# Kernel optimization log

Hardware: AMD Instinct MI355X
Metric: run time of the kernel (lower is better)

The kernel has to match this reference:

```python
import jax, jax.numpy as jnp
import numpy as np

HEAD_NUM = 16
EMBED_DIM = 512


def setup_inputs() -> dict:
    key = jax.random.key(0)
    k1, k2, k3, k4, k5 = jax.random.split(key, 5)
    B, N, D = 8, 2048, EMBED_DIM
    x = jax.random.normal(k1, (B, N, D), dtype=jnp.float32)
    dis_matrix = jax.random.uniform(k2, (B, N, N), dtype=jnp.float32)
    s = 1.0 / np.sqrt(D)
    Wq = jax.random.normal(k3, (D, D), dtype=jnp.float32) * s
    Wk = jax.random.normal(k4, (D, D), dtype=jnp.float32) * s
    Wv = jax.random.normal(k5, (D, D), dtype=jnp.float32) * s
    alpha = jnp.float32(1.0)
    return {"x": x, "dis_matrix": dis_matrix, "Wq": Wq, "Wk": Wk, "Wv": Wv, "alpha": alpha}


def _split_heads(t, H):
    # [B, N, D] -> [B, H, N, D//H]
    B, N, D = t.shape
    return t.reshape(B, N, H, D // H).transpose(0, 2, 1, 3)


def reference(x, dis_matrix, Wq, Wk, Wv, alpha):
    B, N, D = x.shape
    H = HEAD_NUM
    # nn.Linear(bias=False): y = x @ W.T
    q = _split_heads(x @ Wq.T, H)  # [B,H,N,dk]
    k = _split_heads(x @ Wk.T, H)
    v = _split_heads(x @ Wv.T, H)
    log2n = jnp.float32(np.log2(N))
    dis_weight = jnp.exp(-alpha * log2n * dis_matrix)  # [B,N,N]
    k_weight = jnp.exp(k)
    # contract over source node i -> target node j
    weight_1 = jnp.einsum('bij,bhik->bhjk', dis_weight, k_weight * v)
    weight_2 = jnp.einsum('bij,bhik->bhjk', dis_weight, k_weight)
    out = jax.nn.sigmoid(q) * (weight_1 / weight_2)  # [B,H,N,dk]
    return out.transpose(0, 2, 1, 3).reshape(B, N, D)
```

## Files before the change

kernel.cpp:

```cpp
#include <hip/hip_runtime.h>
#include <math.h>
#include <stdint.h>


typedef __bf16 bf16_t;
typedef __attribute__((ext_vector_type(4))) __bf16 bf16x4;
typedef __attribute__((ext_vector_type(8))) __bf16 bf16x8;
typedef __attribute__((ext_vector_type(4))) float f32x4;

#define MFMA_BF16(a, b, c) __builtin_amdgcn_mfma_f32_16x16x32_bf16((a), (b), (c), 0, 0, 0)

static __device__ __forceinline__ void async_ld16(const bf16_t* g, bf16_t* lds) {
  __builtin_amdgcn_global_load_lds(
      reinterpret_cast<__attribute__((address_space(1))) unsigned int*>(
          reinterpret_cast<uintptr_t>(g)),
      reinterpret_cast<__attribute__((address_space(3))) unsigned int*>(
          reinterpret_cast<uintptr_t>(lds)),
      16, 0, 0);
}

template <int BK, int ROWS>
static __device__ __forceinline__ void stage(const bf16_t* g, int ldg, bf16_t* lds,
                                             int wv, int lane) {
  constexpr int CH = BK / 8;
  constexpr int RPW = 64 / CH;
  const int r_in = lane / CH;
  const int cpos = lane % CH;
#pragma unroll
  for (int s = 0; s < ROWS / (RPW * 4); ++s) {
    int rbase = wv * (ROWS / 4) + s * RPW;
    int row = rbase + r_in;
    int cg = cpos ^ ((row >> 1) & 3);
    async_ld16(g + (size_t)row * ldg + cg * 8, lds + rbase * BK + lane * 8);
  }
}

template <int BK>
static __device__ __forceinline__ bf16x8 frag_read(const bf16_t* lds, int row16,
                                                   int l15, int quad, int kc) {
  int p = (quad ^ ((l15 >> 1) & 3)) + kc * 4;
  return *(const bf16x8*)&lds[(row16 + l15) * BK + p * 8];
}

__global__ __launch_bounds__(256) void cvt_all(const float* __restrict__ x,
                                               const float* __restrict__ wq,
                                               const float* __restrict__ wk,
                                               const float* __restrict__ wv,
                                               bf16_t* __restrict__ xb,
                                               bf16_t* __restrict__ wall) {
  int i = blockIdx.x * 256 + threadIdx.x;
  if (i >= 2293760) return;
  const float* src;
  bf16_t* dst;
  int off;
  if (i < 2097152) {
    src = x; dst = xb; off = i;
  } else {
    int j = i - 2097152;
    int sel = j >> 16;
    off = j & 65535;
    src = (sel == 0) ? wq : (sel == 1) ? wk : wv;
    dst = wall + (size_t)sel * 262144;
  }
  f32x4 f = ((const f32x4*)src)[off];
  bf16x4 o;
  o[0] = (bf16_t)f[0]; o[1] = (bf16_t)f[1]; o[2] = (bf16_t)f[2]; o[3] = (bf16_t)f[3];
  ((bf16x4*)dst)[off] = o;
}

__global__ __launch_bounds__(256, 4) void proj_gemm(const bf16_t* __restrict__ A,
                                                    const bf16_t* __restrict__ W,
                                                    bf16_t* __restrict__ qs,
                                                    bf16_t* __restrict__ kwT,
                                                    bf16_t* __restrict__ kwvT) {
  __shared__ __align__(16) char pool[17408];
  bf16_t* As = (bf16_t*)pool;
  const int K = 512;
  const int tid = threadIdx.x;
  const int wv = tid >> 6, lane = tid & 63;
  const int l15 = lane & 15, quad = lane >> 4;
  const int m_blk = blockIdx.x, n_blk = blockIdx.y;
  const int wm = wv >> 1, wn = wv & 1;
  const bf16_t* Am = A + (size_t)(m_blk * 128) * K;

  if (n_blk < 4) {
    bf16_t* Bsq = (bf16_t*)(pool + 8192);
    const int c_loc = n_blk * 128;
    f32x4 acc[4][4];
#pragma unroll
    for (int a = 0; a < 4; ++a)
#pragma unroll
      for (int b = 0; b < 4; ++b) acc[a][b] = (f32x4){0.f, 0.f, 0.f, 0.f};

    for (int k0 = 0; k0 < K; k0 += 32) {
      stage<32, 128>(Am + k0, K, As, wv, lane);
      stage<32, 128>(W + (size_t)c_loc * K + k0, K, Bsq, wv, lane);
      __syncthreads();
      bf16x8 a[4], bb[4];
#pragma unroll
      for (int mf = 0; mf < 4; ++mf) a[mf] = frag_read<32>(As, wm * 64 + mf * 16, l15, quad, 0);
#pragma unroll
      for (int nf = 0; nf < 4; ++nf) bb[nf] = frag_read<32>(Bsq, wn * 64 + nf * 16, l15, quad, 0);
#pragma unroll
      for (int mf = 0; mf < 4; ++mf)
#pragma unroll
        for (int nf = 0; nf < 4; ++nf) acc[mf][nf] = MFMA_BF16(a[mf], bb[nf], acc[mf][nf]);
      __syncthreads();
    }
#pragma unroll
    for (int mf = 0; mf < 4; ++mf)
#pragma unroll
      for (int nf = 0; nf < 4; ++nf) {
        int c = c_loc + wn * 64 + nf * 16 + l15;
#pragma unroll
        for (int r = 0; r < 4; ++r) {
          int t = m_blk * 128 + wm * 64 + mf * 16 + quad * 4 + r;
          qs[(size_t)t * 512 + c] = (bf16_t)(1.0f / (1.0f + __expf(-acc[mf][nf][r])));
        }
      }
  } else {
    bf16_t* Bk = (bf16_t*)(pool + 8192);
    bf16_t* Bv = (bf16_t*)(pool + 12288);
    const int c_loc = (n_blk - 4) * 64;
    f32x4 acck[4][2], accv[4][2];
#pragma unroll
    for (int a = 0; a < 4; ++a)
#pragma unroll
      for (int b = 0; b < 2; ++b) {
        acck[a][b] = (f32x4){0.f, 0.f, 0.f, 0.f};
        accv[a][b] = (f32x4){0.f, 0.f, 0.f, 0.f};
      }
    const bf16_t* Wk = W + (size_t)(512 + c_loc) * K;
    const bf16_t* Wv = W + (size_t)(1024 + c_loc) * K;

    for (int k0 = 0; k0 < K; k0 += 32) {
      stage<32, 128>(Am + k0, K, As, wv, lane);
      stage<32, 64>(Wk + k0, K, Bk, wv, lane);
      stage<32, 64>(Wv + k0, K, Bv, wv, lane);
      __syncthreads();
      bf16x8 a[4], bk[2], bv[2];
#pragma unroll
      for (int mf = 0; mf < 4; ++mf) a[mf] = frag_read<32>(As, wm * 64 + mf * 16, l15, quad, 0);
#pragma unroll
      for (int nf = 0; nf < 2; ++nf) {
        bk[nf] = frag_read<32>(Bk, wn * 32 + nf * 16, l15, quad, 0);
        bv[nf] = frag_read<32>(Bv, wn * 32 + nf * 16, l15, quad, 0);
      }
#pragma unroll
      for (int mf = 0; mf < 4; ++mf)
#pragma unroll
        for (int nf = 0; nf < 2; ++nf) {
          acck[mf][nf] = MFMA_BF16(a[mf], bk[nf], acck[mf][nf]);
          accv[mf][nf] = MFMA_BF16(a[mf], bv[nf], accv[mf][nf]);
        }
      __syncthreads();
    }

    bf16_t* Lk = (bf16_t*)pool;
    bf16_t* Lv = (bf16_t*)(pool + 8704);
    const int bb = m_blk >> 4;
    const int t0 = (m_blk * 128) & 2047;
#pragma unroll
    for (int ci = 0; ci < 2; ++ci) {
      if (wn == ci) {
#pragma unroll
        for (int mf = 0; mf < 4; ++mf)
#pragma unroll
          for (int nf = 0; nf < 2; ++nf) {
            int cl = nf * 16 + l15;
            int tl = wm * 64 + mf * 16 + quad * 4;
#pragma unroll
            for (int r = 0; r < 4; ++r) {
              float kw = __expf(acck[mf][nf][r]);
              Lk[cl * 136 + tl + r] = (bf16_t)kw;
              Lv[cl * 136 + tl + r] = (bf16_t)(kw * accv[mf][nf][r]);
            }
          }
      }
      __syncthreads();
      {
        int rowt = tid >> 3, colt = (tid & 7) * 16;
        int c = c_loc + ci * 32 + rowt;
        size_t g = ((size_t)bb * 512 + c) * 2048 + t0 + colt;
        *(bf16x8*)&kwT[g] = *(const bf16x8*)&Lk[rowt * 136 + colt];
        *(bf16x8*)&kwT[g + 8] = *(const bf16x8*)&Lk[rowt * 136 + colt + 8];
        *(bf16x8*)&kwvT[g] = *(const bf16x8*)&Lv[rowt * 136 + colt];
        *(bf16x8*)&kwvT[g + 8] = *(const bf16x8*)&Lv[rowt * 136 + colt + 8];
      }
      __syncthreads();
    }
  }
}

__global__ __launch_bounds__(256) void make_dwT(const float* __restrict__ dis,
                                                bf16_t* __restrict__ dwT,
                                                const float* __restrict__ alpha) {
  __shared__ bf16_t t[64 * 65];
  const float coef = -alpha[0] * 11.0f;
  const int j0 = blockIdx.x * 64, i0 = blockIdx.y * 64, b = blockIdx.z;
  const int tid = threadIdx.x;
  const int rr = tid >> 4, cc = (tid & 15) * 4;
#pragma unroll
  for (int p = 0; p < 4; ++p) {
    int i = rr + p * 16;
    f32x4 d = *(const f32x4*)&dis[((size_t)(b * 2048 + i0 + i)) * 2048 + j0 + cc];
#pragma unroll
    for (int e = 0; e < 4; ++e) t[(cc + e) * 65 + i] = (bf16_t)__expf(coef * d[e]);
  }
  __syncthreads();
#pragma unroll
  for (int p = 0; p < 4; ++p) {
    int j = rr + p * 16;
    bf16x4 o;
#pragma unroll
    for (int e = 0; e < 4; ++e) o[e] = t[j * 65 + cc + e];
    *(bf16x4*)&dwT[((size_t)(b * 2048 + j0 + j)) * 2048 + i0 + cc] = o;
  }
}

__global__ __launch_bounds__(256, 4) void main_gemm(const bf16_t* __restrict__ dwT,
                                                    const bf16_t* __restrict__ kwvT,
                                                    const bf16_t* __restrict__ kwT,
                                                    const bf16_t* __restrict__ qs,
                                                    float* __restrict__ out) {
  __shared__ bf16_t As[128 * 64];
  __shared__ bf16_t Bs[128 * 64];
  const int K = 2048;
  const int tid = threadIdx.x;
  const int wv = tid >> 6, lane = tid & 63;
  const int l15 = lane & 15, quad = lane >> 4;
  const int i = blockIdx.x;
  const int b = i & 7, nb = (i >> 3) & 7, mb = i >> 6;
  const int wm = wv >> 1, wn = wv & 1;

  const bf16_t* Ab = dwT + ((size_t)b * 2048 + mb * 128) * K;
  const bf16_t* Bv = kwvT + ((size_t)b * 512 + nb * 64) * K;
  const bf16_t* Bk = kwT + ((size_t)b * 512 + nb * 64) * K;
  const int r_in8 = lane >> 3, cpos8 = lane & 7;

  f32x4 acc[4][4];
#pragma unroll
  for (int a = 0; a < 4; ++a)
#pragma unroll
    for (int c = 0; c < 4; ++c) acc[a][c] = (f32x4){0.f, 0.f, 0.f, 0.f};

  for (int k0 = 0; k0 < K; k0 += 64) {
    stage<64, 128>(Ab + k0, K, As, wv, lane);
#pragma unroll
    for (int s = 0; s < 4; ++s) {
      int rbase = wv * 32 + s * 8;
      int row = rbase + r_in8;
      int type = (rbase >> 4) & 1;
      int c = ((rbase >> 5) << 4) + (row & 15);
      int cg = cpos8 ^ ((row >> 1) & 3);
      const bf16_t* src = type ? Bk : Bv;
      async_ld16(src + (size_t)c * K + k0 + cg * 8, Bs + rbase * 64 + lane * 8);
    }
    __syncthreads();
#pragma unroll
    for (int kc = 0; kc < 2; ++kc) {
      bf16x8 a[4], bb[4];
#pragma unroll
      for (int mf = 0; mf < 4; ++mf) a[mf] = frag_read<64>(As, wm * 64 + mf * 16, l15, quad, kc);
#pragma unroll
      for (int nf = 0; nf < 4; ++nf) bb[nf] = frag_read<64>(Bs, wn * 64 + nf * 16, l15, quad, kc);
#pragma unroll
      for (int mf = 0; mf < 4; ++mf)
#pragma unroll
        for (int nf = 0; nf < 4; ++nf) acc[mf][nf] = MFMA_BF16(a[mf], bb[nf], acc[mf][nf]);
    }
    __syncthreads();
  }

#pragma unroll
  for (int mf = 0; mf < 4; ++mf)
#pragma unroll
    for (int p = 0; p < 2; ++p) {
      f32x4 w1 = acc[mf][2 * p];
      f32x4 w2 = acc[mf][2 * p + 1];
      int c = nb * 64 + (wn * 2 + p) * 16 + l15;
#pragma unroll
      for (int r = 0; r < 4; ++r) {
        int j = mb * 128 + wm * 64 + mf * 16 + quad * 4 + r;
        size_t idx = ((size_t)b * 2048 + j) * 512 + c;
        out[idx] = (float)qs[idx] * (w1[r] / w2[r]);
      }
    }
}

extern "C" void kernel_launch(void* const* d_in, const int* in_sizes, int n_in,
                              void* d_out, int out_size, void* d_ws, size_t ws_size,
                              hipStream_t stream) {
  const float* x = (const float*)d_in[0];
  const float* dis = (const float*)d_in[1];
  const float* Wq = (const float*)d_in[2];
  const float* Wk = (const float*)d_in[3];
  const float* Wv = (const float*)d_in[4];
  const float* alpha = (const float*)d_in[5];
  float* out = (float*)d_out;

  char* p = (char*)d_ws;
  bf16_t* x_bf = (bf16_t*)p;  p += (size_t)16384 * 512 * 2;
  bf16_t* Wall = (bf16_t*)p;  p += (size_t)1536 * 512 * 2;
  bf16_t* kwT  = (bf16_t*)p;  p += (size_t)8 * 512 * 2048 * 2;
  bf16_t* kwvT = (bf16_t*)p;  p += (size_t)8 * 512 * 2048 * 2;
  bf16_t* dwT  = (bf16_t*)p;  p += (size_t)8 * 2048 * 2048 * 2;
  bf16_t* qs_bf = (bf16_t*)p; p += (size_t)16384 * 512 * 2;
  if ((size_t)(p - (char*)d_ws) > ws_size) return;

  cvt_all<<<8960, 256, 0, stream>>>(x, Wq, Wk, Wv, x_bf, Wall);
  proj_gemm<<<dim3(128, 12), 256, 0, stream>>>(x_bf, Wall, qs_bf, kwT, kwvT);
  make_dwT<<<dim3(32, 32, 8), 256, 0, stream>>>(dis, dwT, alpha);
  main_gemm<<<1024, 256, 0, stream>>>(dwT, kwvT, kwT, qs_bf, out);
}
```

Before: 358.9 us.

## Fuse projection GEMM and distance-weight transpose into one interleaved launch

Merges the projection GEMM and the dis-matrix exp/transpose kernel into a single launch. Blocks are interleaved 3 GEMM tiles to 16 transpose tiles so the compute-bound and memory-bound work overlap on the GPU. It also raises the projection K-tile from 32 to 64, halving loop iterations and barriers at the cost of more LDS per block. Finally it stores the sigmoid(q) output in a fragment-blocked layout so the main GEMM epilogue reads it with one vector load. The larger shared-memory pool (32KB) applies to every block and may reduce occupancy for the transpose blocks.

```diff
diff --git a/kernel.cpp b/kernel.cpp
--- a/kernel.cpp
+++ b/kernel.cpp
@@ -68,97 +68,138 @@
   ((bf16x4*)dst)[off] = o;
 }
 
-__global__ __launch_bounds__(256, 4) void proj_gemm(const bf16_t* __restrict__ A,
-                                                    const bf16_t* __restrict__ W,
-                                                    bf16_t* __restrict__ qs,
-                                                    bf16_t* __restrict__ kwT,
-                                                    bf16_t* __restrict__ kwvT) {
-  __shared__ __align__(16) char pool[17408];
+__global__ __launch_bounds__(256, 4) void proj_dw(const bf16_t* __restrict__ A,
+                                                  const bf16_t* __restrict__ W,
+                                                  bf16_t* __restrict__ qs,
+                                                  bf16_t* __restrict__ kwT,
+                                                  bf16_t* __restrict__ kwvT,
+                                                  const float* __restrict__ dis,
+                                                  bf16_t* __restrict__ dwT,
+                                                  const float* __restrict__ alpha) {
+  __shared__ __align__(16) char pool[32768];
+  const int tid = threadIdx.x;
+  const int idx = blockIdx.x;
+  const int g19 = idx / 19, r19 = idx % 19;
+
+  if (r19 >= 3) {
+    int sub = g19 * 16 + (r19 - 3);
+    int jt = sub & 31, it = (sub >> 5) & 31, b = sub >> 10;
+    bf16_t* t = (bf16_t*)pool;
+    const float coef = -alpha[0] * 11.0f;
+    const int j0 = jt * 64, i0 = it * 64;
+    const int rr = tid >> 4, cc = (tid & 15) * 4;
+#pragma unroll
+    for (int p = 0; p < 4; ++p) {
+      int i = rr + p * 16;
+      f32x4 d = *(const f32x4*)&dis[((size_t)(b * 2048 + i0 + i)) * 2048 + j0 + cc];
+#pragma unroll
+      for (int e = 0; e < 4; ++e) t[(cc + e) * 65 + i] = (bf16_t)__expf(coef * d[e]);
+    }
+    __syncthreads();
+#pragma unroll
+    for (int p = 0; p < 4; ++p) {
+      int j = rr + p * 16;
+      bf16x4 o;
+#pragma unroll
+      for (int e = 0; e < 4; ++e) o[e] = t[j * 65 + cc + e];
+      *(bf16x4*)&dwT[((size_t)(b * 2048 + j0 + j)) * 2048 + i0 + cc] = o;
+    }
+    return;
+  }
+
+  const int sub = g19 * 3 + r19;
+  const int m_blk = sub / 12, n_blk = sub % 12;
   bf16_t* As = (bf16_t*)pool;
   const int K = 512;
-  const int tid = threadIdx.x;
   const int wv = tid >> 6, lane = tid & 63;
   const int l15 = lane & 15, quad = lane >> 4;
-  const int m_blk = blockIdx.x, n_blk = blockIdx.y;
   const int wm = wv >> 1, wn = wv & 1;
   const bf16_t* Am = A + (size_t)(m_blk * 128) * K;
+  const int b = m_blk >> 4;
 
   if (n_blk < 4) {
-    bf16_t* Bsq = (bf16_t*)(pool + 8192);
+    bf16_t* Bsq = (bf16_t*)(pool + 16384);
     const int c_loc = n_blk * 128;
     f32x4 acc[4][4];
 #pragma unroll
     for (int a = 0; a < 4; ++a)
 #pragma unroll
-      for (int b = 0; b < 4; ++b) acc[a][b] = (f32x4){0.f, 0.f, 0.f, 0.f};
-
-    for (int k0 = 0; k0 < K; k0 += 32) {
-      stage<32, 128>(Am + k0, K, As, wv, lane);
-      stage<32, 128>(W + (size_t)c_loc * K + k0, K, Bsq, wv, lane);
-      __syncthreads();
-      bf16x8 a[4], bb[4];
-#pragma unroll
-      for (int mf = 0; mf < 4; ++mf) a[mf] = frag_read<32>(As, wm * 64 + mf * 16, l15, quad, 0);
-#pragma unroll
-      for (int nf = 0; nf < 4; ++nf) bb[nf] = frag_read<32>(Bsq, wn * 64 + nf * 16, l15, quad, 0);
-#pragma unroll
-      for (int mf = 0; mf < 4; ++mf)
-#pragma unroll
-        for (int nf = 0; nf < 4; ++nf) acc[mf][nf] = MFMA_BF16(a[mf], bb[nf], acc[mf][nf]);
+      for (int c = 0; c < 4; ++c) acc[a][c] = (f32x4){0.f, 0.f, 0.f, 0.f};
+
+    for (int k0 = 0; k0 < K; k0 += 64) {
+      stage<64, 128>(Am + k0, K, As, wv, lane);
+      stage<64, 128>(W + (size_t)c_loc * K + k0, K, Bsq, wv, lane);
+      __syncthreads();
+#pragma unroll
+      for (int kc = 0; kc < 2; ++kc) {
+        bf16x8 a[4], bb[4];
+#pragma unroll
+        for (int mf = 0; mf < 4; ++mf) a[mf] = frag_read<64>(As, wm * 64 + mf * 16, l15, quad, kc);
+#pragma unroll
+        for (int nf = 0; nf < 4; ++nf) bb[nf] = frag_read<64>(Bsq, wn * 64 + nf * 16, l15, quad, kc);
+#pragma unroll
+        for (int mf = 0; mf < 4; ++mf)
+#pragma unroll
+          for (int nf = 0; nf < 4; ++nf) acc[mf][nf] = MFMA_BF16(a[mf], bb[nf], acc[mf][nf]);
+      }
       __syncthreads();
     }
 #pragma unroll
     for (int mf = 0; mf < 4; ++mf)
 #pragma unroll
       for (int nf = 0; nf < 4; ++nf) {
-        int c = c_loc + wn * 64 + nf * 16 + l15;
-#pragma unroll
-        for (int r = 0; r < 4; ++r) {
-          int t = m_blk * 128 + wm * 64 + mf * 16 + quad * 4 + r;
-          qs[(size_t)t * 512 + c] = (bf16_t)(1.0f / (1.0f + __expf(-acc[mf][nf][r])));
-        }
+        int j16 = (m_blk & 15) * 8 + wm * 4 + mf;
+        int c16 = n_blk * 8 + wn * 4 + nf;
+        bf16x4 o;
+#pragma unroll
+        for (int r = 0; r < 4; ++r)
+          o[r] = (bf16_t)(1.0f / (1.0f + __expf(-acc[mf][nf][r])));
+        size_t off = (((size_t)b * 128 + j16) * 32 + c16) * 256 + quad * 64 + l15 * 4;
+        *(bf16x4*)&qs[off] = o;
       }
   } else {
-    bf16_t* Bk = (bf16_t*)(pool + 8192);
-    bf16_t* Bv = (bf16_t*)(pool + 12288);
+    bf16_t* Bk = (bf16_t*)(pool + 16384);
+    bf16_t* Bv = (bf16_t*)(pool + 24576);
     const int c_loc = (n_blk - 4) * 64;
     f32x4 acck[4][2], accv[4][2];
 #pragma unroll
     for (int a = 0; a < 4; ++a)
 #pragma unroll
-      for (int b = 0; b < 2; ++b) {
-        acck[a][b] = (f32x4){0.f, 0.f, 0.f, 0.f};
-        accv[a][b] = (f32x4){0.f, 0.f, 0.f, 0.f};
+      for (int c = 0; c < 2; ++c) {
+        acck[a][c] = (f32x4){0.f, 0.f, 0.f, 0.f};
+        accv[a][c] = (f32x4){0.f, 0.f, 0.f, 0.f};
       }
     const bf16_t* Wk = W + (size_t)(512 + c_loc) * K;
     const bf16_t* Wv = W + (size_t)(1024 + c_loc) * K;
 
-    for (int k0 = 0; k0 < K; k0 += 32) {
-      stage<32, 128>(Am + k0, K, As, wv, lane);
-      stage<32, 64>(Wk + k0, K, Bk, wv, lane);
-      stage<32, 64>(Wv + k0, K, Bv, wv, lane);
-      __syncthreads();
-      bf16x8 a[4], bk[2], bv[2];
-#pragma unroll
-      for (int mf = 0; mf < 4; ++mf) a[mf] = frag_read<32>(As, wm * 64 + mf * 16, l15, quad, 0);
-#pragma unroll
-      for (int nf = 0; nf < 2; ++nf) {
-        bk[nf] = frag_read<32>(Bk, wn * 32 + nf * 16, l15, quad, 0);
-        bv[nf] = frag_read<32>(Bv, wn * 32 + nf * 16, l15, quad, 0);
-      }
-#pragma unroll
-      for (int mf = 0; mf < 4; ++mf)
+    for (int k0 = 0; k0 < K; k0 += 64) {
+      stage<64, 128>(Am + k0, K, As, wv, lane);
+      stage<64, 64>(Wk + k0, K, Bk, wv, lane);
+      stage<64, 64>(Wv + k0, K, Bv, wv, lane);
+      __syncthreads();
+#pragma unroll
+      for (int kc = 0; kc < 2; ++kc) {
+        bf16x8 a[4], bk[2], bv[2];
+#pragma unroll
+        for (int mf = 0; mf < 4; ++mf) a[mf] = frag_read<64>(As, wm * 64 + mf * 16, l15, quad, kc);
 #pragma unroll
         for (int nf = 0; nf < 2; ++nf) {
-          acck[mf][nf] = MFMA_BF16(a[mf], bk[nf], acck[mf][nf]);
-          accv[mf][nf] = MFMA_BF16(a[mf], bv[nf], accv[mf][nf]);
+          bk[nf] = frag_read<64>(Bk, wn * 32 + nf * 16, l15, quad, kc);
+          bv[nf] = frag_read<64>(Bv, wn * 32 + nf * 16, l15, quad, kc);
         }
+#pragma unroll
+        for (int mf = 0; mf < 4; ++mf)
+#pragma unroll
+          for (int nf = 0; nf < 2; ++nf) {
+            acck[mf][nf] = MFMA_BF16(a[mf], bk[nf], acck[mf][nf]);
+            accv[mf][nf] = MFMA_BF16(a[mf], bv[nf], accv[mf][nf]);
+          }
+      }
       __syncthreads();
     }
 
     bf16_t* Lk = (bf16_t*)pool;
     bf16_t* Lv = (bf16_t*)(pool + 8704);
-    const int bb = m_blk >> 4;
     const int t0 = (m_blk * 128) & 2047;
 #pragma unroll
     for (int ci = 0; ci < 2; ++ci) {
@@ -181,7 +222,7 @@
       {
         int rowt = tid >> 3, colt = (tid & 7) * 16;
         int c = c_loc + ci * 32 + rowt;
-        size_t g = ((size_t)bb * 512 + c) * 2048 + t0 + colt;
+        size_t g = ((size_t)b * 512 + c) * 2048 + t0 + colt;
         *(bf16x8*)&kwT[g] = *(const bf16x8*)&Lk[rowt * 136 + colt];
         *(bf16x8*)&kwT[g + 8] = *(const bf16x8*)&Lk[rowt * 136 + colt + 8];
         *(bf16x8*)&kwvT[g] = *(const bf16x8*)&Lv[rowt * 136 + colt];
@@ -189,32 +230,6 @@
       }
       __syncthreads();
     }
-  }
-}
-
-__global__ __launch_bounds__(256) void make_dwT(const float* __restrict__ dis,
-                                                bf16_t* __restrict__ dwT,
-                                                const float* __restrict__ alpha) {
-  __shared__ bf16_t t[64 * 65];
-  const float coef = -alpha[0] * 11.0f;
-  const int j0 = blockIdx.x * 64, i0 = blockIdx.y * 64, b = blockIdx.z;
-  const int tid = threadIdx.x;
-  const int rr = tid >> 4, cc = (tid & 15) * 4;
-#pragma unroll
-  for (int p = 0; p < 4; ++p) {
-    int i = rr + p * 16;
-    f32x4 d = *(const f32x4*)&dis[((size_t)(b * 2048 + i0 + i)) * 2048 + j0 + cc];
-#pragma unroll
-    for (int e = 0; e < 4; ++e) t[(cc + e) * 65 + i] = (bf16_t)__expf(coef * d[e]);
-  }
-  __syncthreads();
-#pragma unroll
-  for (int p = 0; p < 4; ++p) {
-    int j = rr + p * 16;
-    bf16x4 o;
-#pragma unroll
-    for (int e = 0; e < 4; ++e) o[e] = t[j * 65 + cc + e];
-    *(bf16x4*)&dwT[((size_t)(b * 2048 + j0 + j)) * 2048 + i0 + cc] = o;
   }
 }
 
@@ -278,12 +293,16 @@
     for (int p = 0; p < 2; ++p) {
       f32x4 w1 = acc[mf][2 * p];
       f32x4 w2 = acc[mf][2 * p + 1];
+      int j16 = mb * 8 + wm * 4 + mf;
+      int c16 = nb * 4 + wn * 2 + p;
+      size_t qoff = (((size_t)b * 128 + j16) * 32 + c16) * 256 + quad * 64 + l15 * 4;
+      bf16x4 qv = *(const bf16x4*)&qs[qoff];
       int c = nb * 64 + (wn * 2 + p) * 16 + l15;
 #pragma unroll
       for (int r = 0; r < 4; ++r) {
         int j = mb * 128 + wm * 64 + mf * 16 + quad * 4 + r;
         size_t idx = ((size_t)b * 2048 + j) * 512 + c;
-        out[idx] = (float)qs[idx] * (w1[r] / w2[r]);
+        out[idx] = (float)qv[r] * (w1[r] / w2[r]);
       }
     }
 }
@@ -309,7 +328,6 @@
   if ((size_t)(p - (char*)d_ws) > ws_size) return;
 
   cvt_all<<<8960, 256, 0, stream>>>(x, Wq, Wk, Wv, x_bf, Wall);
-  proj_gemm<<<dim3(128, 12), 256, 0, stream>>>(x_bf, Wall, qs_bf, kwT, kwvT);
-  make_dwT<<<dim3(32, 32, 8), 256, 0, stream>>>(dis, dwT, alpha);
+  proj_dw<<<9728, 256, 0, stream>>>(x_bf, Wall, qs_bf, kwT, kwvT, dis, dwT, alpha);
   main_gemm<<<1024, 256, 0, stream>>>(dwT, kwvT, kwT, qs_bf, out);
 }
```

Measured after the change: 349.5 us. 2.6% less time.
